# Kernel tuning notes

Hardware: AMD Instinct MI355X
Metric: run time of the kernel (lower is better)

Reference implementation:

```python
import jax, jax.numpy as jnp
import numpy as np

# Static config matching init_kwargs / input_specs
B, CIN, H, W = 4, 64, 128, 128
COUT, K, DG = 64, 3, 8
STRIDE, PAD, DIL = 1, 1, 1
HO = (H + 2 * PAD - DIL * (K - 1) - 1) // STRIDE + 1
WO = (W + 2 * PAD - DIL * (K - 1) - 1) // STRIDE + 1
KK = K * K
CG = CIN // DG  # channels per deformable group


def setup_inputs() -> dict:
    key = jax.random.key(0)
    k1, k2, k3, k4 = jax.random.split(key, 4)
    x = jax.random.normal(k1, (B, CIN, H, W), jnp.float32)
    offset = jax.random.normal(k2, (B, 2 * DG * KK, HO, WO), jnp.float32)
    s = 1.0 / np.sqrt(CIN * KK)  # matches reset_parameters stdv / fan_in bound
    weight = jax.random.uniform(k3, (COUT, CIN, K, K), jnp.float32, -s, s)
    bias = jax.random.uniform(k4, (COUT,), jnp.float32, -s, s)
    return {"x": x, "offset": offset, "weight": weight, "bias": bias}


def _deform_conv(x, offset, weight, bias):
    # offset layout (DCNv1): [B, DG * KK * 2, Ho, Wo], per kernel point (dy, dx)
    off = offset.reshape(B, DG, KK, 2, HO, WO)
    khs = (jnp.repeat(jnp.arange(K), K) * DIL).astype(jnp.float32)  # [KK] kernel dy
    kws = (jnp.tile(jnp.arange(K), K) * DIL).astype(jnp.float32)    # [KK] kernel dx
    gy = (jnp.arange(HO) * STRIDE - PAD).astype(jnp.float32)        # [Ho] base y
    gx = (jnp.arange(WO) * STRIDE - PAD).astype(jnp.float32)        # [Wo] base x
    # sampling positions: [B, DG, KK, Ho, Wo]
    py = gy[None, None, None, :, None] + khs[None, None, :, None, None] + off[:, :, :, 0]
    px = gx[None, None, None, None, :] + kws[None, None, :, None, None] + off[:, :, :, 1]
    y0 = jnp.floor(py)
    x0 = jnp.floor(px)
    ly = py - y0  # fractional parts
    lx = px - x0
    xg = x.reshape(B, DG, CG, H * W)  # channels grouped by deformable group

    def corner(yc, xc, wgt):
        # zero-padded bilinear: out-of-bounds corners contribute 0
        valid = (yc >= 0) & (yc < H) & (xc >= 0) & (xc < W)
        idx = (jnp.clip(yc, 0, H - 1) * W + jnp.clip(xc, 0, W - 1)).astype(jnp.int32)
        v = jnp.take_along_axis(xg, idx.reshape(B, DG, 1, KK * HO * WO), axis=3)
        v = v.reshape(B, DG, CG, KK, HO, WO)
        w = jnp.where(valid, wgt, 0.0)  # [B, DG, KK, Ho, Wo]
        return v * w[:, :, None]

    cols = (corner(y0, x0, (1.0 - ly) * (1.0 - lx))
            + corner(y0, x0 + 1.0, (1.0 - ly) * lx)
            + corner(y0 + 1.0, x0, ly * (1.0 - lx))
            + corner(y0 + 1.0, x0 + 1.0, ly * lx))  # [B, DG, CG, KK, Ho, Wo]

    wk = weight.reshape(COUT, DG, CG, KK)  # groups == 1
    out = jnp.einsum('bgcpyx,ogcp->boyx', cols, wk)
    return out + bias[None, :, None, None]


def reference(x, offset, weight, bias):
    return _deform_conv(x, offset, weight, bias)
```

## Files before the change

kernel.cpp:

```cpp
#include <hip/hip_runtime.h>

#define BB    4
#define CINT  64
#define HH    128
#define WW    128
#define COUTN 64
#define DGN   8
#define CGN   8
#define KKN   9
#define HOWO  16384
#define HWSZ  (HH * WW)
#define HP    132
#define WP    132
#define HWP   (HP * WP)
#define NXG   (BB * DGN * HWP)
#define NCHUNK 18
#define NWBLK  18

typedef __bf16 bf16x8 __attribute__((ext_vector_type(8)));
typedef float  f32x4  __attribute__((ext_vector_type(4)));

static __device__ __forceinline__ ushort f2bf(float f) {
    unsigned u = __builtin_bit_cast(unsigned, f);
    u += 0x7fffu + ((u >> 16) & 1u);
    return (ushort)(u >> 16);
}

__global__ __launch_bounds__(256) void prep(
    const float* __restrict__ x, const float* __restrict__ wgt,
    uint4* __restrict__ xh, uint4* __restrict__ wq)
{
    const int bid = blockIdx.x;
    const int tid = threadIdx.x;
    if (bid < NWBLK) {
        int i = bid * 256 + tid;
        int lane = i & 63;
        int mt   = (i >> 6) & 3;
        int kt   = i >> 8;
        int m = lane & 15, quad = lane >> 4;
        int o = mt * 16 + m;
        union { ushort u[8]; uint4 v; } pk;
#pragma unroll
        for (int j = 0; j < 8; ++j) {
            int k   = kt * 32 + quad * 8 + j;
            int gkk = k >> 3, c = k & 7;
            int g   = gkk / 9, kk = gkk - 9 * g;
            pk.u[j] = f2bf(wgt[(o * CINT + g * CGN + c) * KKN + kk]);
        }
        wq[i] = pk.v;
        return;
    }
    int j = (bid - NWBLK) * 256 + tid;
    if (j >= NXG) return;
    int bg = j / HWP;
    int r  = j - bg * HWP;
    int yp = r / WP;
    int xp = r - yp * WP;
    union { ushort u[8]; uint4 v; } pk;
    pk.v.x = pk.v.y = pk.v.z = pk.v.w = 0u;
    if (yp >= 2 && yp <= 129 && xp >= 2 && xp <= 129) {
        const float* src = x + (size_t)bg * CGN * HWSZ + (yp - 2) * WW + (xp - 2);
#pragma unroll
        for (int c = 0; c < CGN; ++c) pk.u[c] = f2bf(src[c * HWSZ]);
    }
    xh[j] = pk.v;
}

__global__ __launch_bounds__(256, 4) void dcn_mfma(
    const uint4* __restrict__ xh, const float* __restrict__ off,
    const uint4* __restrict__ wq, const float* __restrict__ bias,
    float* __restrict__ out)
{
    const int tid  = threadIdx.x;
    const int wave = tid >> 6;
    const int lane = tid & 63;
    const int q    = lane >> 4;
    const int n    = lane & 15;

    const int wid     = blockIdx.x * 4 + wave;
    const int pixbase = wid * 16;
    const int b       = pixbase >> 14;
    const int rem     = (pixbase & 16383) + n;
    const int ho = rem >> 7, wo = rem & 127;
    const float fy0 = (float)(ho - 1);
    const float fx0 = (float)(wo - 1);

    const float* offp = off + (size_t)(b * 72 + q) * 2 * HOWO + rem;

    float lofy[4], lofx[4];
#pragma unroll
    for (int c0 = 0; c0 < 4; ++c0) {
        lofy[c0] = offp[(size_t)c0 * 8 * HOWO];
        lofx[c0] = offp[(size_t)c0 * 8 * HOWO + HOWO];
    }

    f32x4 acc[4];
#pragma unroll
    for (int mt = 0; mt < 4; ++mt) acc[mt] = (f32x4){0.f, 0.f, 0.f, 0.f};

    const int xbase = b * DGN * HWP;

    int g = 0, kk = q;
    uint4 c00, c01, c10, c11, n00, n01, n10, n11;
    float w00, w01, w10, w11, v00, v01, v10, v11;

    auto issue = [&](int ch, uint4& r00, uint4& r01, uint4& r10, uint4& r11,
                     float& u00, float& u01, float& u10, float& u11) {
        int kh = (kk * 11) >> 5;
        int kw = kk - 3 * kh;
        float py  = fy0 + (float)kh + lofy[ch & 3];
        float pxx = fx0 + (float)kw + lofx[ch & 3];
        float y0f = floorf(py), x0f = floorf(pxx);
        float ly = py - y0f, lx = pxx - x0f;
        float hy = 1.f - ly, hx = 1.f - lx;
        u00 = hy * hx; u01 = hy * lx; u10 = ly * hx; u11 = ly * lx;
        int y0 = (int)y0f, x0 = (int)x0f;
        y0 = min(max(y0, -2), HH);
        x0 = min(max(x0, -2), WW);
        const uint4* p = xh + (xbase + g * HWP + (y0 + 2) * WP + (x0 + 2));
        r00 = p[0]; r01 = p[1]; r10 = p[WP]; r11 = p[WP + 1];
        kk += 4; if (kk >= KKN) { kk -= KKN; ++g; }
    };

    issue(0, c00, c01, c10, c11, w00, w01, w10, w11);

#pragma unroll
    for (int ch = 0; ch < NCHUNK; ++ch) {
        if (ch + 4 < NCHUNK) {
            lofy[(ch + 4) & 3] = offp[(size_t)(ch + 4) * 8 * HOWO];
            lofx[(ch + 4) & 3] = offp[(size_t)(ch + 4) * 8 * HOWO + HOWO];
        }
        if (ch + 1 < NCHUNK)
            issue(ch + 1, n00, n01, n10, n11, v00, v01, v10, v11);

        const __bf16* a00 = (const __bf16*)&c00;
        const __bf16* a01 = (const __bf16*)&c01;
        const __bf16* a10 = (const __bf16*)&c10;
        const __bf16* a11 = (const __bf16*)&c11;
        bf16x8 bfrag;
#pragma unroll
        for (int cc = 0; cc < 8; ++cc) {
            float v = w00 * (float)a00[cc] + w01 * (float)a01[cc]
                    + w10 * (float)a10[cc] + w11 * (float)a11[cc];
            bfrag[cc] = (__bf16)v;
        }
#pragma unroll
        for (int mt = 0; mt < 4; ++mt) {
            bf16x8 afrag = __builtin_bit_cast(bf16x8, wq[(ch * 4 + mt) * 64 + lane]);
            acc[mt] = __builtin_amdgcn_mfma_f32_16x16x32_bf16(afrag, bfrag, acc[mt], 0, 0, 0);
        }
        if (ch + 1 < NCHUNK) {
            c00 = n00; c01 = n01; c10 = n10; c11 = n11;
            w00 = v00; w01 = v01; w10 = v10; w11 = v11;
        }
    }

    const int rem_out = (pixbase & 16383) + n;
    float* outp = out + (size_t)b * COUTN * HOWO + rem_out;
#pragma unroll
    for (int mt = 0; mt < 4; ++mt) {
        f32x4 bv = *(const f32x4*)(bias + mt * 16 + q * 4);
#pragma unroll
        for (int r = 0; r < 4; ++r) {
            int o = mt * 16 + q * 4 + r;
            outp[(size_t)o * HOWO] = acc[mt][r] + bv[r];
        }
    }
}

extern "C" void kernel_launch(void* const* d_in, const int* in_sizes, int n_in,
                              void* d_out, int out_size, void* d_ws, size_t ws_size,
                              hipStream_t stream) {
    const float* x    = (const float*)d_in[0];
    const float* off  = (const float*)d_in[1];
    const float* wgt  = (const float*)d_in[2];
    const float* bias = (const float*)d_in[3];
    float* out = (float*)d_out;

    uint4* xh = (uint4*)d_ws;
    uint4* wq = (uint4*)((char*)d_ws + (size_t)NXG * 16);

    const int xblocks = (NXG + 255) / 256;
    prep<<<dim3(NWBLK + xblocks), dim3(256), 0, stream>>>(x, wgt, xh, wq);
    dcn_mfma<<<dim3(BB * HOWO / 64), dim3(256), 0, stream>>>(xh, off, wq, bias, out);
}
```

Measured before the change: 123.3 us.

## Split reduction across two waves per pixel tile with LDS combine

Each 16-pixel tile is now handled by two waves, each covering half of the 18 K-chunks, and the partial accumulators are summed through shared memory before the output write. The grid doubles and the launch bound asks for higher occupancy, so there are more waves available to hide gather latency on the bilinear loads. The cost is an LDS round trip, a block-wide barrier, and half the waves sitting idle during the epilogue.

```diff
diff --git a/kernel.cpp b/kernel.cpp
--- a/kernel.cpp
+++ b/kernel.cpp
@@ -15,6 +15,7 @@
 #define HWP   (HP * WP)
 #define NXG   (BB * DGN * HWP)
 #define NCHUNK 18
+#define NCHALF 9
 #define NWBLK  18
 
 typedef __bf16 bf16x8 __attribute__((ext_vector_type(8)));
@@ -66,26 +67,30 @@
     xh[j] = pk.v;
 }
 
-__global__ __launch_bounds__(256, 4) void dcn_mfma(
+__global__ __launch_bounds__(256, 8) void dcn_mfma(
     const uint4* __restrict__ xh, const float* __restrict__ off,
     const uint4* __restrict__ wq, const float* __restrict__ bias,
     float* __restrict__ out)
 {
+    __shared__ f32x4 lred[2][4][64];
+
     const int tid  = threadIdx.x;
     const int wave = tid >> 6;
     const int lane = tid & 63;
+    const int tile = wave >> 1;
+    const int half = wave & 1;
+    const int ch0  = half * NCHALF;
     const int q    = lane >> 4;
     const int n    = lane & 15;
 
-    const int wid     = blockIdx.x * 4 + wave;
-    const int pixbase = wid * 16;
+    const int pixbase = blockIdx.x * 32 + tile * 16;
     const int b       = pixbase >> 14;
     const int rem     = (pixbase & 16383) + n;
     const int ho = rem >> 7, wo = rem & 127;
     const float fy0 = (float)(ho - 1);
     const float fx0 = (float)(wo - 1);
 
-    const float* offp = off + (size_t)(b * 72 + q) * 2 * HOWO + rem;
+    const float* offp = off + (size_t)(b * 72 + ch0 * 4 + q) * 2 * HOWO + rem;
 
     float lofy[4], lofx[4];
 #pragma unroll
@@ -100,16 +105,17 @@
 
     const int xbase = b * DGN * HWP;
 
-    int g = 0, kk = q;
+    const int gkk0 = ch0 * 4 + q;
+    int g = gkk0 / KKN, kk = gkk0 - KKN * (gkk0 / KKN);
     uint4 c00, c01, c10, c11, n00, n01, n10, n11;
     float w00, w01, w10, w11, v00, v01, v10, v11;
 
-    auto issue = [&](int ch, uint4& r00, uint4& r01, uint4& r10, uint4& r11,
+    auto issue = [&](int cc, uint4& r00, uint4& r01, uint4& r10, uint4& r11,
                      float& u00, float& u01, float& u10, float& u11) {
         int kh = (kk * 11) >> 5;
         int kw = kk - 3 * kh;
-        float py  = fy0 + (float)kh + lofy[ch & 3];
-        float pxx = fx0 + (float)kw + lofx[ch & 3];
+        float py  = fy0 + (float)kh + lofy[cc & 3];
+        float pxx = fx0 + (float)kw + lofx[cc & 3];
         float y0f = floorf(py), x0f = floorf(pxx);
         float ly = py - y0f, lx = pxx - x0f;
         float hy = 1.f - ly, hx = 1.f - lx;
@@ -125,13 +131,13 @@
     issue(0, c00, c01, c10, c11, w00, w01, w10, w11);
 
 #pragma unroll
-    for (int ch = 0; ch < NCHUNK; ++ch) {
-        if (ch + 4 < NCHUNK) {
-            lofy[(ch + 4) & 3] = offp[(size_t)(ch + 4) * 8 * HOWO];
-            lofx[(ch + 4) & 3] = offp[(size_t)(ch + 4) * 8 * HOWO + HOWO];
-        }
-        if (ch + 1 < NCHUNK)
-            issue(ch + 1, n00, n01, n10, n11, v00, v01, v10, v11);
+    for (int cc = 0; cc < NCHALF; ++cc) {
+        if (cc + 4 < NCHALF) {
+            lofy[(cc + 4) & 3] = offp[(size_t)(cc + 4) * 8 * HOWO];
+            lofx[(cc + 4) & 3] = offp[(size_t)(cc + 4) * 8 * HOWO + HOWO];
+        }
+        if (cc + 1 < NCHALF)
+            issue(cc + 1, n00, n01, n10, n11, v00, v01, v10, v11);
 
         const __bf16* a00 = (const __bf16*)&c00;
         const __bf16* a01 = (const __bf16*)&c01;
@@ -139,20 +145,34 @@
         const __bf16* a11 = (const __bf16*)&c11;
         bf16x8 bfrag;
 #pragma unroll
-        for (int cc = 0; cc < 8; ++cc) {
-            float v = w00 * (float)a00[cc] + w01 * (float)a01[cc]
-                    + w10 * (float)a10[cc] + w11 * (float)a11[cc];
-            bfrag[cc] = (__bf16)v;
+        for (int ccc = 0; ccc < 8; ++ccc) {
+            float v = w00 * (float)a00[ccc] + w01 * (float)a01[ccc]
+                    + w10 * (float)a10[ccc] + w11 * (float)a11[ccc];
+            bfrag[ccc] = (__bf16)v;
         }
 #pragma unroll
         for (int mt = 0; mt < 4; ++mt) {
-            bf16x8 afrag = __builtin_bit_cast(bf16x8, wq[(ch * 4 + mt) * 64 + lane]);
+            bf16x8 afrag = __builtin_bit_cast(bf16x8, wq[((ch0 + cc) * 4 + mt) * 64 + lane]);
             acc[mt] = __builtin_amdgcn_mfma_f32_16x16x32_bf16(afrag, bfrag, acc[mt], 0, 0, 0);
         }
-        if (ch + 1 < NCHUNK) {
+        if (cc + 1 < NCHALF) {
             c00 = n00; c01 = n01; c10 = n10; c11 = n11;
             w00 = v00; w01 = v01; w10 = v10; w11 = v11;
         }
+    }
+
+    if (half == 1) {
+#pragma unroll
+        for (int mt = 0; mt < 4; ++mt) lred[tile][mt][lane] = acc[mt];
+    }
+    __syncthreads();
+    if (half == 1) return;
+
+#pragma unroll
+    for (int mt = 0; mt < 4; ++mt) {
+        f32x4 pv = lred[tile][mt][lane];
+        acc[mt][0] += pv[0]; acc[mt][1] += pv[1];
+        acc[mt][2] += pv[2]; acc[mt][3] += pv[3];
     }
 
     const int rem_out = (pixbase & 16383) + n;
@@ -182,5 +202,5 @@
 
     const int xblocks = (NXG + 255) / 256;
     prep<<<dim3(NWBLK + xblocks), dim3(256), 0, stream>>>(x, wgt, xh, wq);
-    dcn_mfma<<<dim3(BB * HOWO / 64), dim3(256), 0, stream>>>(xh, off, wq, bias, out);
-}
+    dcn_mfma<<<dim3(BB * HOWO / 32), dim3(256), 0, stream>>>(xh, off, wq, bias, out);
+}
```

Measured after the change: 123.1 us. About the same (-0.1%).
